# Performance work log

Hardware: AMD Instinct MI355X
Metric: run time of the kernel (lower is better)

## Reference

```python
import jax, jax.numpy as jnp
import numpy as np

EPS = 1e-5

def _relu6(x):
    return jnp.clip(x, 0.0, 6.0)

def _bn(x, g, b, m, v):
    # inference-mode batchnorm folded into scale/shift
    inv = g / jnp.sqrt(v + EPS)
    return x * inv[None, :, None, None] + (b - m * inv)[None, :, None, None]

def _patch_pw(x, W):
    # per-patch 1x1 conv. x: [B,Ci,H,Wd], W: [B,Fh,Fw,Co,Ci]
    B, C, H, Wd = x.shape
    Fh, Fw = W.shape[1:3]
    ph, pw = H // Fh, Wd // Fw
    xb = x.reshape(B, C, Fh, ph, Fw, pw)
    yb = jnp.einsum('bfgoc,bcfpgq->bofpgq', W, xb)
    return yb.reshape(B, W.shape[3], H, Wd)

def _patch_dw3(x, K):
    # per-patch depthwise 3x3, reflect pad applied to the full map (halo from neighbors).
    # x: [B,C,H,Wd], K: [B,Fh,Fw,C,3,3]
    B, C, H, Wd = x.shape
    Fh, Fw = K.shape[1:3]
    ph, pw = H // Fh, Wd // Fw
    xp = jnp.pad(x, ((0, 0), (0, 0), (1, 1), (1, 1)), mode='reflect')
    acc = jnp.zeros((B, C, Fh, ph, Fw, pw), x.dtype)
    for dy in range(3):
        for dx in range(3):
            xs = xp[:, :, dy:dy + H, dx:dx + Wd].reshape(B, C, Fh, ph, Fw, pw)
            k = K[:, :, :, :, dy, dx].transpose(0, 3, 1, 2)  # [B,C,Fh,Fw]
            acc = acc + xs * k[:, :, :, None, :, None]
    return acc.reshape(B, C, H, Wd)

def setup_inputs() -> dict:
    key = jax.random.key(0)
    ks = jax.random.split(key, 16)
    B, Cin, H, Wd = 4, 64, 128, 128
    hidden, Cout, Fh, Fw = 384, 64, 16, 16
    n_params = hidden * Cin + hidden * 9 + Cout * hidden  # 52608
    return {
        'x': jax.random.normal(ks[0], (B, Cin, H, Wd), jnp.float32),
        'w': jax.random.normal(ks[1], (B, n_params, Fh, Fw), jnp.float32) * 0.05,
        'g1': jax.random.uniform(ks[2], (hidden,), jnp.float32),
        'b1': jax.random.normal(ks[3], (hidden,), jnp.float32),
        'm1': jax.random.normal(ks[4], (hidden,), jnp.float32),
        'v1': jax.random.uniform(ks[5], (hidden,), jnp.float32),
        'g2': jax.random.uniform(ks[6], (hidden,), jnp.float32),
        'b2': jax.random.normal(ks[7], (hidden,), jnp.float32),
        'm2': jax.random.normal(ks[8], (hidden,), jnp.float32),
        'v2': jax.random.uniform(ks[9], (hidden,), jnp.float32),
        'g3': jax.random.uniform(ks[10], (Cout,), jnp.float32),
        'b3': jax.random.normal(ks[11], (Cout,), jnp.float32),
        'm3': jax.random.normal(ks[12], (Cout,), jnp.float32),
        'v3': jax.random.uniform(ks[13], (Cout,), jnp.float32),
    }

def reference(x, w, g1, b1, m1, v1, g2, b2, m2, v2, g3, b3, m3, v3):
    B, Cin = x.shape[:2]
    Fh, Fw = w.shape[2:]
    hidden = g1.shape[0]
    Cout = g3.shape[0]
    n1 = hidden * Cin
    n2 = hidden * 9
    wg = w.transpose(0, 2, 3, 1)  # [B,Fh,Fw,P]
    W1 = wg[..., :n1].reshape(B, Fh, Fw, hidden, Cin)
    K2 = wg[..., n1:n1 + n2].reshape(B, Fh, Fw, hidden, 3, 3)
    W3 = wg[..., n1 + n2:].reshape(B, Fh, Fw, Cout, hidden)
    h = _relu6(_bn(_patch_pw(x, W1), g1, b1, m1, v1))
    h = _relu6(_bn(_patch_dw3(h, K2), g2, b2, m2, v2))
    h = _bn(_patch_pw(h, W3), g3, b3, m3, v3)
    return x + h  # use_res_connect: stride==1 and in_nc==out_nc
```

## Files before the change

kernel.cpp:

```cpp
#include <hip/hip_runtime.h>

#define EPSV 1e-5f

constexpr int CIN = 64, NH = 128, NW = 128, HID = 384, COUT = 64;
constexpr int N1 = HID * CIN;
constexpr int N2 = HID * 9;
constexpr int NP = N1 + N2 + COUT * HID;

using bf16x8 = __attribute__((ext_vector_type(8))) short;
using f32x4  = __attribute__((ext_vector_type(4))) float;
using h16x2  = __attribute__((ext_vector_type(2))) _Float16;
using f16x8  = __attribute__((ext_vector_type(8))) _Float16;

__device__ __forceinline__ unsigned short f2bf(float f) {
  unsigned int u = __float_as_uint(f);
  u = (u + 0x7fffu + ((u >> 16) & 1u)) >> 16;
  return (unsigned short)u;
}
__device__ __forceinline__ unsigned int pack2(float a, float b) {
  return (unsigned int)f2bf(a) | ((unsigned int)f2bf(b) << 16);
}
__device__ __forceinline__ unsigned int pkh2(float a, float b) {
  auto h = __builtin_amdgcn_cvt_pkrtz(a, b);
  return *reinterpret_cast<unsigned int*>(&h);
}
__device__ __forceinline__ unsigned short f2h(float f) {
  _Float16 h = (_Float16)f;
  return *reinterpret_cast<unsigned short*>(&h);
}
__device__ __forceinline__ h16x2 uh2(unsigned int u) {
  return *reinterpret_cast<h16x2*>(&u);
}
__device__ __forceinline__ float clamp6(float v) { return fminf(fmaxf(v, 0.f), 6.f); }

#define BAR_LDS()                                             \
  do {                                                        \
    asm volatile("s_waitcnt lgkmcnt(0)" ::: "memory");        \
    __builtin_amdgcn_s_barrier();                             \
  } while (0)

__global__ __launch_bounds__(256) void k0_transpose(
    const float* __restrict__ x, unsigned short* __restrict__ xT) {
  __shared__ unsigned short xls[64][66];
  const int t = threadIdx.x;
  const int xh = blockIdx.x, y = blockIdx.y, b = blockIdx.z;
#pragma unroll
  for (int it = 0; it < 4; ++it) {
    int i = it * 256 + t;
    int xq = i & 15, c = i >> 4;
    float4 v = *reinterpret_cast<const float4*>(
        &x[((size_t)(b * CIN + c) * NH + y) * NW + xh * 64 + xq * 4]);
    *(unsigned int*)&xls[c][xq * 4]     = pack2(v.x, v.y);
    *(unsigned int*)&xls[c][xq * 4 + 2] = pack2(v.z, v.w);
  }
  __syncthreads();
#pragma unroll
  for (int it = 0; it < 4; ++it) {
    int i = it * 256 + t;
    int cq = i & 15, px = i >> 4;
    ushort4 o;
    o.x = xls[cq * 4 + 0][px];
    o.y = xls[cq * 4 + 1][px];
    o.z = xls[cq * 4 + 2][px];
    o.w = xls[cq * 4 + 3][px];
    *reinterpret_cast<ushort4*>(
        &xT[((size_t)(b * NH + y) * NW + xh * 64 + px) * 64 + cq * 4]) = o;
  }
}

__global__ __launch_bounds__(256) void k1_pw1(
    const float* __restrict__ w, const unsigned short* __restrict__ xT,
    const float* __restrict__ g1, const float* __restrict__ b1,
    const float* __restrict__ m1, const float* __restrict__ v1,
    unsigned short* __restrict__ h1T) {
  __shared__ unsigned short Wpk[2048 * 8];

  const unsigned int id = blockIdx.x;
  const int fbq = id & 7;
  const unsigned int rest = id >> 3;
  const int hgrp = rest % 24, q = rest / 24;
  const int fb = q * 8 + fbq;
  const int f = fb & 15, b = fb >> 4;
  const int h0 = hgrp * 16;

  const int t = threadIdx.x;
  const int lane = t & 63, wv = t >> 6;
  const int quad = lane >> 4, nn = lane & 15;
  const int pxi = wv * 16 + nn;

#pragma unroll
  for (int it = 0; it < 8; ++it) {
    int i = it * 256 + t;
    int gq = i & 3, cp = (i >> 2) & 31, hid = i >> 7;
    const float* wp =
        &w[((size_t)b * NP + (h0 + hid) * CIN + cp * 2) * 256 + f * 16 + gq * 4];
    float4 A  = *reinterpret_cast<const float4*>(wp);
    float4 Bv = *reinterpret_cast<const float4*>(wp + 256);
    int kc = cp >> 4, qd = (cp >> 2) & 3, j = (cp & 3) * 2;
    int hs = hid ^ (2 * qd) ^ gq;
    const float* Af = (const float*)&A;
    const float* Bf = (const float*)&Bv;
#pragma unroll
    for (int k = 0; k < 4; ++k) {
      int g = gq * 4 + k;
      *(unsigned int*)&Wpk[(((g * 2 + kc) * 4 + qd) * 16 + hs) * 8 + j] =
          pack2(Af[k], Bf[k]);
    }
  }

  float iv1[4], sh1[4];
#pragma unroll
  for (int jj = 0; jj < 4; ++jj) {
    int hid = h0 + quad * 4 + jj;
    float iv = g1[hid] * rsqrtf(v1[hid] + EPSV);
    iv1[jj] = iv;
    sh1[jj] = b1[hid] - m1[hid] * iv;
  }
  __syncthreads();

  const int y = f * 8 + (pxi >> 3);
  const size_t rowbase = ((size_t)b * NH + y) * NW;

  for (int g = 0; g < 16; ++g) {
    const int xc = g * 8 + (pxi & 7);
    const unsigned short* xp = &xT[(rowbase + xc) * 64];
    f32x4 acc = {0.f, 0.f, 0.f, 0.f};
    const int hs = nn ^ (2 * quad) ^ (g >> 2);
#pragma unroll
    for (int kc = 0; kc < 2; ++kc) {
      bf16x8 af = *reinterpret_cast<const bf16x8*>(
          &Wpk[(((g * 2 + kc) * 4 + quad) * 16 + hs) * 8]);
      bf16x8 bfr = *reinterpret_cast<const bf16x8*>(&xp[kc * 32 + quad * 8]);
      acc = __builtin_amdgcn_mfma_f32_16x16x32_bf16(af, bfr, acc, 0, 0, 0);
    }
    uint2 o;
    o.x = pkh2(clamp6(acc[0] * iv1[0] + sh1[0]),
               clamp6(acc[1] * iv1[1] + sh1[1]));
    o.y = pkh2(clamp6(acc[2] * iv1[2] + sh1[2]),
               clamp6(acc[3] * iv1[3] + sh1[3]));
    *reinterpret_cast<uint2*>(&h1T[(rowbase + xc) * HID + h0 + quad * 4]) = o;
  }
}

__global__ __launch_bounds__(256, 2) void k2_fused(
    const float* __restrict__ x, const float* __restrict__ w,
    const float* __restrict__ g2, const float* __restrict__ b2v,
    const float* __restrict__ m2, const float* __restrict__ v2,
    const float* __restrict__ g3, const float* __restrict__ b3v,
    const float* __restrict__ m3, const float* __restrict__ v3,
    const unsigned short* __restrict__ h1T, float* __restrict__ out) {
  __shared__ unsigned short tile[10][34][40];
  __shared__ unsigned short h2s[256][40];
  __shared__ unsigned short W3p[512 * 8];
  __shared__ unsigned short k2w[4][9][40];
  __shared__ float iv2s[HID], sh2s[HID];

  const unsigned int id = blockIdx.x;
  const int fbq = id & 7;
  const unsigned int rest = id >> 3;
  const int gang = rest & 7, q = rest >> 3;
  const int fb = q * 8 + fbq;
  const int f = fb & 15, b = fb >> 4;
  const int gq = gang >> 1, ch = gang & 1;
  const int c0 = gq * 32;

  const int t = threadIdx.x;
  const int lane = t & 63, wv = t >> 6;
  const int quad = lane >> 4, nn = lane & 15;

  for (int i = t; i < HID; i += 256) {
    float iv = g2[i] * rsqrtf(v2[i] + EPSV);
    iv2s[i] = iv;
    sh2s[i] = b2v[i] - m2[i] * iv;
  }

  float iv3[2][4], sh3[2][4];
#pragma unroll
  for (int cot = 0; cot < 2; ++cot)
#pragma unroll
    for (int jj = 0; jj < 4; ++jj) {
      int co = ch * 32 + cot * 16 + quad * 4 + jj;
      float iv = g3[co] * rsqrtf(v3[co] + EPSV);
      iv3[cot][jj] = iv;
      sh3[cot][jj] = b3v[co] - m3[co] * iv;
    }

  f32x4 acc[2][4];
#pragma unroll
  for (int cot = 0; cot < 2; ++cot)
#pragma unroll
    for (int nt = 0; nt < 4; ++nt) acc[cot][nt] = (f32x4){0.f, 0.f, 0.f, 0.f};

  const int glt = t >> 6, rt = (t >> 3) & 7, ct = t & 7;

#define TGEOM(IDX, SRC, DST)                                          \
  {                                                                   \
    int qh = (IDX) & 3, pxid = (IDX) >> 2;                            \
    int r = pxid / 34, col = pxid - r * 34;                           \
    int yy = f * 8 - 1 + r;                                           \
    yy = (yy < 0) ? -yy : ((yy > 127) ? 254 - yy : yy);               \
    int xc = c0 - 1 + col;                                            \
    xc = (xc < 0) ? 1 : ((xc > 127) ? 126 : xc);                      \
    SRC = &h1T[(((size_t)b * NH + yy) * NW + xc) * HID + qh * 8];     \
    DST = &tile[r][col][qh * 8];                                      \
  }
  const unsigned short *ts0, *ts1, *ts2, *ts3, *ts4, *ts5;
  unsigned short *td0, *td1, *td2, *td3, *td4, *td5;
  const bool tac5 = (t < 80);
  TGEOM(t, ts0, td0);
  TGEOM(256 + t, ts1, td1);
  TGEOM(512 + t, ts2, td2);
  TGEOM(768 + t, ts3, td3);
  TGEOM(1024 + t, ts4, td4);
  {
    int idx5 = tac5 ? (1280 + t) : 1359;
    TGEOM(idx5, ts5, td5);
  }
#undef TGEOM

  const int hh1 = t / 9, tap1 = t - hh1 * 9;
  const float* ksrc1 = &w[((size_t)b * NP + N1 + t) * 256 + f * 16 + gq * 4];
  const bool kac2 = (t < 32);
  const int i2k = 256 + t;
  const int hh2 = i2k / 9, tap2 = i2k - hh2 * 9;
  const float* ksrc2 = &w[((size_t)b * NP + N1 + i2k) * 256 + f * 16 + gq * 4];

  const float *wsrc0, *wsrc1;
  unsigned int *wd00, *wd01, *wd02, *wd03, *wd10, *wd11, *wd12, *wd13;
#define W3GEOM(IT, SRC, D0, D1, D2, D3)                                   \
  {                                                                      \
    int i = (IT) * 256 + t;                                              \
    int hhp = i & 15, co = i >> 4;                                       \
    SRC = &w[((size_t)b * NP + N1 + N2 + (ch * 32 + co) * HID + hhp * 2) * \
                 256 + f * 16 + gq * 4];                                 \
    int qd = (hhp * 2) >> 3, j = (hhp * 2) & 7, cot = co >> 4,           \
        cb = co & 15;                                                    \
    D0 = (unsigned int*)&W3p[(((0 * 2 + cot) * 4 + qd) * 16 +            \
                              (cb ^ (2 * qd) ^ 0)) * 8 + j];             \
    D1 = (unsigned int*)&W3p[(((1 * 2 + cot) * 4 + qd) * 16 +            \
                              (cb ^ (2 * qd) ^ 1)) * 8 + j];             \
    D2 = (unsigned int*)&W3p[(((2 * 2 + cot) * 4 + qd) * 16 +            \
                              (cb ^ (2 * qd) ^ 2)) * 8 + j];             \
    D3 = (unsigned int*)&W3p[(((3 * 2 + cot) * 4 + qd) * 16 +            \
                              (cb ^ (2 * qd) ^ 3)) * 8 + j];             \
  }
  W3GEOM(0, wsrc0, wd00, wd01, wd02, wd03);
  W3GEOM(1, wsrc1, wd10, wd11, wd12, wd13);
#undef W3GEOM

  uint4 tr0, tr1, tr2, tr3, tr4, tr5;
  float4 kr1, kr2;
  float4 wA0, wB0, wA1, wB1;

#define PREFETCH()                                                  \
  do {                                                              \
    tr0 = *reinterpret_cast<const uint4*>(ts0); ts0 += 32;          \
    tr1 = *reinterpret_cast<const uint4*>(ts1); ts1 += 32;          \
    tr2 = *reinterpret_cast<const uint4*>(ts2); ts2 += 32;          \
    tr3 = *reinterpret_cast<const uint4*>(ts3); ts3 += 32;          \
    tr4 = *reinterpret_cast<const uint4*>(ts4); ts4 += 32;          \
    if (tac5) tr5 = *reinterpret_cast<const uint4*>(ts5);           \
    ts5 += 32;                                                      \
    kr1 = *reinterpret_cast<const float4*>(ksrc1); ksrc1 += 73728;  \
    if (kac2) kr2 = *reinterpret_cast<const float4*>(ksrc2);        \
    ksrc2 += 73728;                                                 \
    wA0 = *reinterpret_cast<const float4*>(wsrc0);                  \
    wB0 = *reinterpret_cast<const float4*>(wsrc0 + 256);            \
    wsrc0 += 8192;                                                  \
    wA1 = *reinterpret_cast<const float4*>(wsrc1);                  \
    wB1 = *reinterpret_cast<const float4*>(wsrc1 + 256);            \
    wsrc1 += 8192;                                                  \
  } while (0)

  tr5 = (uint4){0u, 0u, 0u, 0u};
  kr2 = (float4){0.f, 0.f, 0.f, 0.f};
  PREFETCH();

  const h16x2 hz = {(_Float16)0.f, (_Float16)0.f};

  for (int hc = 0; hc < 12; ++hc) {
    const int hb = hc * 32;
    BAR_LDS();

    *reinterpret_cast<uint4*>(td0) = tr0;
    *reinterpret_cast<uint4*>(td1) = tr1;
    *reinterpret_cast<uint4*>(td2) = tr2;
    *reinterpret_cast<uint4*>(td3) = tr3;
    *reinterpret_cast<uint4*>(td4) = tr4;
    if (tac5) *reinterpret_cast<uint4*>(td5) = tr5;
    k2w[0][tap1][hh1] = f2h(kr1.x);
    k2w[1][tap1][hh1] = f2h(kr1.y);
    k2w[2][tap1][hh1] = f2h(kr1.z);
    k2w[3][tap1][hh1] = f2h(kr1.w);
    if (kac2) {
      k2w[0][tap2][hh2] = f2h(kr2.x);
      k2w[1][tap2][hh2] = f2h(kr2.y);
      k2w[2][tap2][hh2] = f2h(kr2.z);
      k2w[3][tap2][hh2] = f2h(kr2.w);
    }
    *wd00 = pkh2(wA0.x, wB0.x);
    *wd01 = pkh2(wA0.y, wB0.y);
    *wd02 = pkh2(wA0.z, wB0.z);
    *wd03 = pkh2(wA0.w, wB0.w);
    *wd10 = pkh2(wA1.x, wB1.x);
    *wd11 = pkh2(wA1.y, wB1.y);
    *wd12 = pkh2(wA1.z, wB1.z);
    *wd13 = pkh2(wA1.w, wB1.w);

    BAR_LDS();

    if (hc < 11) PREFETCH();

#pragma unroll
    for (int hg = 0; hg < 4; ++hg) {
      h16x2 d0 = hz, d1 = hz, d2 = hz, d3 = hz;
#pragma unroll
      for (int dy = 0; dy < 3; ++dy)
#pragma unroll
        for (int dx = 0; dx < 3; ++dx) {
          const uint4 tv = *reinterpret_cast<const uint4*>(
              &tile[rt + dy][glt * 8 + ct + dx][hg * 8]);
          const uint4 kv =
              *reinterpret_cast<const uint4*>(&k2w[glt][dy * 3 + dx][hg * 8]);
          d0 += uh2(tv.x) * uh2(kv.x);
          d1 += uh2(tv.y) * uh2(kv.y);
          d2 += uh2(tv.z) * uh2(kv.z);
          d3 += uh2(tv.w) * uh2(kv.w);
        }
      const int ha = hb + hg * 8;
      uint4 o4;
      o4.x = pkh2(clamp6((float)d0[0] * iv2s[ha + 0] + sh2s[ha + 0]),
                  clamp6((float)d0[1] * iv2s[ha + 1] + sh2s[ha + 1]));
      o4.y = pkh2(clamp6((float)d1[0] * iv2s[ha + 2] + sh2s[ha + 2]),
                  clamp6((float)d1[1] * iv2s[ha + 3] + sh2s[ha + 3]));
      o4.z = pkh2(clamp6((float)d2[0] * iv2s[ha + 4] + sh2s[ha + 4]),
                  clamp6((float)d2[1] * iv2s[ha + 5] + sh2s[ha + 5]));
      o4.w = pkh2(clamp6((float)d3[0] * iv2s[ha + 6] + sh2s[ha + 6]),
                  clamp6((float)d3[1] * iv2s[ha + 7] + sh2s[ha + 7]));
      *reinterpret_cast<uint4*>(&h2s[t][hg * 8]) = o4;
    }

    BAR_LDS();

    {
      const int gl = wv;
      const int cop = nn ^ (2 * quad) ^ gl;
      f16x8 a0 = *reinterpret_cast<const f16x8*>(
          &W3p[(((gl * 2 + 0) * 4 + quad) * 16 + cop) * 8]);
      f16x8 a1 = *reinterpret_cast<const f16x8*>(
          &W3p[(((gl * 2 + 1) * 4 + quad) * 16 + cop) * 8]);
#pragma unroll
      for (int nt = 0; nt < 4; ++nt) {
        f16x8 bfr = *reinterpret_cast<const f16x8*>(
            &h2s[gl * 64 + nt * 16 + nn][quad * 8]);
        acc[0][nt] = __builtin_amdgcn_mfma_f32_16x16x32_f16(a0, bfr, acc[0][nt], 0, 0, 0);
        acc[1][nt] = __builtin_amdgcn_mfma_f32_16x16x32_f16(a1, bfr, acc[1][nt], 0, 0, 0);
      }
    }
  }

#pragma unroll
  for (int cot = 0; cot < 2; ++cot)
#pragma unroll
    for (int nt = 0; nt < 4; ++nt) {
      int pxl = nt * 16 + nn;
      int y = f * 8 + (pxl >> 3);
      int xc = c0 + wv * 8 + (pxl & 7);
#pragma unroll
      for (int jj = 0; jj < 4; ++jj) {
        int co = ch * 32 + cot * 16 + quad * 4 + jj;
        size_t adr = ((size_t)(b * COUT + co) * NH + y) * NW + xc;
        out[adr] = acc[cot][nt][jj] * iv3[cot][jj] + sh3[cot][jj] + x[adr];
      }
    }
}

extern "C" void kernel_launch(void* const* d_in, const int* in_sizes, int n_in,
                              void* d_out, int out_size, void* d_ws,
                              size_t ws_size, hipStream_t stream) {
  (void)in_sizes; (void)n_in; (void)out_size; (void)ws_size;
  const float* x  = (const float*)d_in[0];
  const float* w  = (const float*)d_in[1];
  const float* g1 = (const float*)d_in[2];
  const float* b1 = (const float*)d_in[3];
  const float* m1 = (const float*)d_in[4];
  const float* v1 = (const float*)d_in[5];
  const float* g2 = (const float*)d_in[6];
  const float* b2 = (const float*)d_in[7];
  const float* m2 = (const float*)d_in[8];
  const float* v2 = (const float*)d_in[9];
  const float* g3 = (const float*)d_in[10];
  const float* b3 = (const float*)d_in[11];
  const float* m3 = (const float*)d_in[12];
  const float* v3 = (const float*)d_in[13];
  float* out = (float*)d_out;
  unsigned short* h1T = (unsigned short*)d_ws;
  unsigned short* xT = (unsigned short*)d_out;

  k0_transpose<<<dim3(2, 128, 4), 256, 0, stream>>>(x, xT);
  k1_pw1<<<dim3(1536), 256, 0, stream>>>(w, xT, g1, b1, m1, v1, h1T);
  k2_fused<<<dim3(512), 256, 0, stream>>>(x, w, g2, b2, m2, v2, g3, b3, m3, v3,
                                          h1T, out);
}
```

Measured before the change: 431.3 us.

## Split k2 block work by spatial rows instead of output channels

Each k2 block now covers a 4-row by 32-column pixel tile and computes all 64 output channels, where before it covered an 8x32 tile and only half the channels. The depthwise 3x3 stage is no longer done twice for the same pixels, and the halo tile and h2s buffers shrink. Each block now stages the full W3 slice (twice as much per block) and has proportionally more halo overhead. LDS use drops enough that launch bounds are raised from 2 to 3 blocks per SIMD for occupancy.

```diff
diff --git a/kernel.cpp b/kernel.cpp
--- a/kernel.cpp
+++ b/kernel.cpp
@@ -142,16 +142,16 @@
   }
 }
 
-__global__ __launch_bounds__(256, 2) void k2_fused(
+__global__ __launch_bounds__(256, 3) void k2_fused(
     const float* __restrict__ x, const float* __restrict__ w,
     const float* __restrict__ g2, const float* __restrict__ b2v,
     const float* __restrict__ m2, const float* __restrict__ v2,
     const float* __restrict__ g3, const float* __restrict__ b3v,
     const float* __restrict__ m3, const float* __restrict__ v3,
     const unsigned short* __restrict__ h1T, float* __restrict__ out) {
-  __shared__ unsigned short tile[10][34][40];
-  __shared__ unsigned short h2s[256][40];
-  __shared__ unsigned short W3p[512 * 8];
+  __shared__ unsigned short tile[6][34][40];
+  __shared__ unsigned short h2s[128][40];
+  __shared__ unsigned short W3p[8192];
   __shared__ unsigned short k2w[4][9][40];
   __shared__ float iv2s[HID], sh2s[HID];
 
@@ -163,10 +163,14 @@
   const int f = fb & 15, b = fb >> 4;
   const int gq = gang >> 1, ch = gang & 1;
   const int c0 = gq * 32;
+  const int r0 = f * 8 + ch * 4;
 
   const int t = threadIdx.x;
   const int lane = t & 63, wv = t >> 6;
   const int quad = lane >> 4, nn = lane & 15;
+  const int glh = wv & 1, coh = wv >> 1;
+  const int p = t & 127, hhalf = t >> 7;
+  const int patchq = p >> 5, prt = (p >> 3) & 3, pct = p & 7;
 
   for (int i = t; i < HID; i += 256) {
     float iv = g2[i] * rsqrtf(v2[i] + EPSV);
@@ -179,7 +183,7 @@
   for (int cot = 0; cot < 2; ++cot)
 #pragma unroll
     for (int jj = 0; jj < 4; ++jj) {
-      int co = ch * 32 + cot * 16 + quad * 4 + jj;
+      int co = coh * 32 + cot * 16 + quad * 4 + jj;
       float iv = g3[co] * rsqrtf(v3[co] + EPSV);
       iv3[cot][jj] = iv;
       sh3[cot][jj] = b3v[co] - m3[co] * iv;
@@ -190,31 +194,27 @@
   for (int cot = 0; cot < 2; ++cot)
 #pragma unroll
     for (int nt = 0; nt < 4; ++nt) acc[cot][nt] = (f32x4){0.f, 0.f, 0.f, 0.f};
-
-  const int glt = t >> 6, rt = (t >> 3) & 7, ct = t & 7;
 
 #define TGEOM(IDX, SRC, DST)                                          \
   {                                                                   \
     int qh = (IDX) & 3, pxid = (IDX) >> 2;                            \
     int r = pxid / 34, col = pxid - r * 34;                           \
-    int yy = f * 8 - 1 + r;                                           \
+    int yy = r0 - 1 + r;                                              \
     yy = (yy < 0) ? -yy : ((yy > 127) ? 254 - yy : yy);               \
     int xc = c0 - 1 + col;                                            \
     xc = (xc < 0) ? 1 : ((xc > 127) ? 126 : xc);                      \
     SRC = &h1T[(((size_t)b * NH + yy) * NW + xc) * HID + qh * 8];     \
     DST = &tile[r][col][qh * 8];                                      \
   }
-  const unsigned short *ts0, *ts1, *ts2, *ts3, *ts4, *ts5;
-  unsigned short *td0, *td1, *td2, *td3, *td4, *td5;
-  const bool tac5 = (t < 80);
+  const unsigned short *ts0, *ts1, *ts2, *ts3;
+  unsigned short *td0, *td1, *td2, *td3;
+  const bool tac3 = (t < 48);
   TGEOM(t, ts0, td0);
   TGEOM(256 + t, ts1, td1);
   TGEOM(512 + t, ts2, td2);
-  TGEOM(768 + t, ts3, td3);
-  TGEOM(1024 + t, ts4, td4);
   {
-    int idx5 = tac5 ? (1280 + t) : 1359;
-    TGEOM(idx5, ts5, td5);
+    int idx3 = tac3 ? (768 + t) : 815;
+    TGEOM(idx3, ts3, td3);
   }
 #undef TGEOM
 
@@ -225,42 +225,37 @@
   const int hh2 = i2k / 9, tap2 = i2k - hh2 * 9;
   const float* ksrc2 = &w[((size_t)b * NP + N1 + i2k) * 256 + f * 16 + gq * 4];
 
-  const float *wsrc0, *wsrc1;
-  unsigned int *wd00, *wd01, *wd02, *wd03, *wd10, *wd11, *wd12, *wd13;
-#define W3GEOM(IT, SRC, D0, D1, D2, D3)                                   \
+  const float *wsrc0, *wsrc1, *wsrc2, *wsrc3;
+  unsigned int wb0, wb1, wb2, wb3;
+#define W3GEOM(IT, SRC, WB)                                               \
   {                                                                      \
     int i = (IT) * 256 + t;                                              \
-    int hhp = i & 15, co = i >> 4;                                       \
-    SRC = &w[((size_t)b * NP + N1 + N2 + (ch * 32 + co) * HID + hhp * 2) * \
-                 256 + f * 16 + gq * 4];                                 \
-    int qd = (hhp * 2) >> 3, j = (hhp * 2) & 7, cot = co >> 4,           \
-        cb = co & 15;                                                    \
-    D0 = (unsigned int*)&W3p[(((0 * 2 + cot) * 4 + qd) * 16 +            \
-                              (cb ^ (2 * qd) ^ 0)) * 8 + j];             \
-    D1 = (unsigned int*)&W3p[(((1 * 2 + cot) * 4 + qd) * 16 +            \
-                              (cb ^ (2 * qd) ^ 1)) * 8 + j];             \
-    D2 = (unsigned int*)&W3p[(((2 * 2 + cot) * 4 + qd) * 16 +            \
-                              (cb ^ (2 * qd) ^ 2)) * 8 + j];             \
-    D3 = (unsigned int*)&W3p[(((3 * 2 + cot) * 4 + qd) * 16 +            \
-                              (cb ^ (2 * qd) ^ 3)) * 8 + j];             \
-  }
-  W3GEOM(0, wsrc0, wd00, wd01, wd02, wd03);
-  W3GEOM(1, wsrc1, wd10, wd11, wd12, wd13);
+    int hhp = i & 15, co = i >> 4;                         \
+    SRC = &w[((size_t)b * NP + N1 + N2 + co * HID + hhp * 2) * 256 +     \
+             f * 16 + gq * 4];                                           \
+    int qd = (hhp * 2) >> 3, j = (hhp * 2) & 7;                          \
+    int ch2 = co >> 5, cot = (co >> 4) & 1, cb = co & 15;                \
+    int cop0 = cb ^ (2 * qd);                                            \
+    WB = (unsigned int)(ch2 * 8192 + (cot * 4 + qd) * 256 + cop0 * 16 +  \
+                        j * 2);                                          \
+  }
+  W3GEOM(0, wsrc0, wb0);
+  W3GEOM(1, wsrc1, wb1);
+  W3GEOM(2, wsrc2, wb2);
+  W3GEOM(3, wsrc3, wb3);
 #undef W3GEOM
 
-  uint4 tr0, tr1, tr2, tr3, tr4, tr5;
+  uint4 tr0, tr1, tr2, tr3;
   float4 kr1, kr2;
-  float4 wA0, wB0, wA1, wB1;
+  float4 wA0, wB0, wA1, wB1, wA2, wB2, wA3, wB3;
 
 #define PREFETCH()                                                  \
   do {                                                              \
     tr0 = *reinterpret_cast<const uint4*>(ts0); ts0 += 32;          \
     tr1 = *reinterpret_cast<const uint4*>(ts1); ts1 += 32;          \
     tr2 = *reinterpret_cast<const uint4*>(ts2); ts2 += 32;          \
-    tr3 = *reinterpret_cast<const uint4*>(ts3); ts3 += 32;          \
-    tr4 = *reinterpret_cast<const uint4*>(ts4); ts4 += 32;          \
-    if (tac5) tr5 = *reinterpret_cast<const uint4*>(ts5);           \
-    ts5 += 32;                                                      \
+    if (tac3) tr3 = *reinterpret_cast<const uint4*>(ts3);           \
+    ts3 += 32;                                                      \
     kr1 = *reinterpret_cast<const float4*>(ksrc1); ksrc1 += 73728;  \
     if (kac2) kr2 = *reinterpret_cast<const float4*>(ksrc2);        \
     ksrc2 += 73728;                                                 \
@@ -270,9 +265,25 @@
     wA1 = *reinterpret_cast<const float4*>(wsrc1);                  \
     wB1 = *reinterpret_cast<const float4*>(wsrc1 + 256);            \
     wsrc1 += 8192;                                                  \
+    wA2 = *reinterpret_cast<const float4*>(wsrc2);                  \
+    wB2 = *reinterpret_cast<const float4*>(wsrc2 + 256);            \
+    wsrc2 += 8192;                                                  \
+    wA3 = *reinterpret_cast<const float4*>(wsrc3);                  \
+    wB3 = *reinterpret_cast<const float4*>(wsrc3 + 256);            \
+    wsrc3 += 8192;                                                  \
   } while (0)
 
-  tr5 = (uint4){0u, 0u, 0u, 0u};
+#define W3WRITE(WB, WA, WV)                                                   \
+  do {                                                                        \
+    const float* Af = (const float*)&(WA);                                    \
+    const float* Bf = (const float*)&(WV);                                    \
+    *(unsigned int*)((char*)W3p + (WB))                  = pkh2(Af[0], Bf[0]);\
+    *(unsigned int*)((char*)W3p + (((WB) ^ 16) + 2048))  = pkh2(Af[1], Bf[1]);\
+    *(unsigned int*)((char*)W3p + (((WB) ^ 32) + 4096))  = pkh2(Af[2], Bf[2]);\
+    *(unsigned int*)((char*)W3p + (((WB) ^ 48) + 6144))  = pkh2(Af[3], Bf[3]);\
+  } while (0)
+
+  tr3 = (uint4){0u, 0u, 0u, 0u};
   kr2 = (float4){0.f, 0.f, 0.f, 0.f};
   PREFETCH();
 
@@ -285,9 +296,7 @@
     *reinterpret_cast<uint4*>(td0) = tr0;
     *reinterpret_cast<uint4*>(td1) = tr1;
     *reinterpret_cast<uint4*>(td2) = tr2;
-    *reinterpret_cast<uint4*>(td3) = tr3;
-    *reinterpret_cast<uint4*>(td4) = tr4;
-    if (tac5) *reinterpret_cast<uint4*>(td5) = tr5;
+    if (tac3) *reinterpret_cast<uint4*>(td3) = tr3;
     k2w[0][tap1][hh1] = f2h(kr1.x);
     k2w[1][tap1][hh1] = f2h(kr1.y);
     k2w[2][tap1][hh1] = f2h(kr1.z);
@@ -298,30 +307,27 @@
       k2w[2][tap2][hh2] = f2h(kr2.z);
       k2w[3][tap2][hh2] = f2h(kr2.w);
     }
-    *wd00 = pkh2(wA0.x, wB0.x);
-    *wd01 = pkh2(wA0.y, wB0.y);
-    *wd02 = pkh2(wA0.z, wB0.z);
-    *wd03 = pkh2(wA0.w, wB0.w);
-    *wd10 = pkh2(wA1.x, wB1.x);
-    *wd11 = pkh2(wA1.y, wB1.y);
-    *wd12 = pkh2(wA1.z, wB1.z);
-    *wd13 = pkh2(wA1.w, wB1.w);
+    W3WRITE(wb0, wA0, wB0);
+    W3WRITE(wb1, wA1, wB1);
+    W3WRITE(wb2, wA2, wB2);
+    W3WRITE(wb3, wA3, wB3);
 
     BAR_LDS();
 
     if (hc < 11) PREFETCH();
 
 #pragma unroll
-    for (int hg = 0; hg < 4; ++hg) {
+    for (int hg2 = 0; hg2 < 2; ++hg2) {
+      const int hg = hhalf * 2 + hg2;
       h16x2 d0 = hz, d1 = hz, d2 = hz, d3 = hz;
 #pragma unroll
       for (int dy = 0; dy < 3; ++dy)
 #pragma unroll
         for (int dx = 0; dx < 3; ++dx) {
           const uint4 tv = *reinterpret_cast<const uint4*>(
-              &tile[rt + dy][glt * 8 + ct + dx][hg * 8]);
+              &tile[prt + dy][patchq * 8 + pct + dx][hg * 8]);
           const uint4 kv =
-              *reinterpret_cast<const uint4*>(&k2w[glt][dy * 3 + dx][hg * 8]);
+              *reinterpret_cast<const uint4*>(&k2w[patchq][dy * 3 + dx][hg * 8]);
           d0 += uh2(tv.x) * uh2(kv.x);
           d1 += uh2(tv.y) * uh2(kv.y);
           d2 += uh2(tv.z) * uh2(kv.z);
@@ -337,24 +343,33 @@
                   clamp6((float)d2[1] * iv2s[ha + 5] + sh2s[ha + 5]));
       o4.w = pkh2(clamp6((float)d3[0] * iv2s[ha + 6] + sh2s[ha + 6]),
                   clamp6((float)d3[1] * iv2s[ha + 7] + sh2s[ha + 7]));
-      *reinterpret_cast<uint4*>(&h2s[t][hg * 8]) = o4;
+      *reinterpret_cast<uint4*>(&h2s[p][hg * 8]) = o4;
     }
 
     BAR_LDS();
 
     {
-      const int gl = wv;
-      const int cop = nn ^ (2 * quad) ^ gl;
-      f16x8 a0 = *reinterpret_cast<const f16x8*>(
-          &W3p[(((gl * 2 + 0) * 4 + quad) * 16 + cop) * 8]);
-      f16x8 a1 = *reinterpret_cast<const f16x8*>(
-          &W3p[(((gl * 2 + 1) * 4 + quad) * 16 + cop) * 8]);
+      const int cop0 = nn ^ (2 * quad);
+      const int kp0 = glh * 2, kp1 = glh * 2 + 1;
+      f16x8 aA0 = *reinterpret_cast<const f16x8*>(
+          &W3p[coh * 4096 + (((kp0 * 2 + 0) * 4 + quad) * 16 + (cop0 ^ kp0)) * 8]);
+      f16x8 aB0 = *reinterpret_cast<const f16x8*>(
+          &W3p[coh * 4096 + (((kp0 * 2 + 1) * 4 + quad) * 16 + (cop0 ^ kp0)) * 8]);
+      f16x8 aA1 = *reinterpret_cast<const f16x8*>(
+          &W3p[coh * 4096 + (((kp1 * 2 + 0) * 4 + quad) * 16 + (cop0 ^ kp1)) * 8]);
+      f16x8 aB1 = *reinterpret_cast<const f16x8*>(
+          &W3p[coh * 4096 + (((kp1 * 2 + 1) * 4 + quad) * 16 + (cop0 ^ kp1)) * 8]);
 #pragma unroll
       for (int nt = 0; nt < 4; ++nt) {
         f16x8 bfr = *reinterpret_cast<const f16x8*>(
-            &h2s[gl * 64 + nt * 16 + nn][quad * 8]);
-        acc[0][nt] = __builtin_amdgcn_mfma_f32_16x16x32_f16(a0, bfr, acc[0][nt], 0, 0, 0);
-        acc[1][nt] = __builtin_amdgcn_mfma_f32_16x16x32_f16(a1, bfr, acc[1][nt], 0, 0, 0);
+            &h2s[glh * 64 + nt * 16 + nn][quad * 8]);
+        if (nt < 2) {
+          acc[0][nt] = __builtin_amdgcn_mfma_f32_16x16x32_f16(aA0, bfr, acc[0][nt], 0, 0, 0);
+          acc[1][nt] = __builtin_amdgcn_mfma_f32_16x16x32_f16(aB0, bfr, acc[1][nt], 0, 0, 0);
+        } else {
+          acc[0][nt] = __builtin_amdgcn_mfma_f32_16x16x32_f16(aA1, bfr, acc[0][nt], 0, 0, 0);
+          acc[1][nt] = __builtin_amdgcn_mfma_f32_16x16x32_f16(aB1, bfr, acc[1][nt], 0, 0, 0);
+        }
       }
     }
   }
@@ -363,12 +378,13 @@
   for (int cot = 0; cot < 2; ++cot)
 #pragma unroll
     for (int nt = 0; nt < 4; ++nt) {
-      int pxl = nt * 16 + nn;
-      int y = f * 8 + (pxl >> 3);
-      int xc = c0 + wv * 8 + (pxl & 7);
+      int rt_ = (nt & 1) * 2 + (nn >> 3);
+      int patch_ = glh * 2 + (nt >> 1);
+      int y = r0 + rt_;
+      int xc = c0 + patch_ * 8 + (nn & 7);
 #pragma unroll
       for (int jj = 0; jj < 4; ++jj) {
-        int co = ch * 32 + cot * 16 + quad * 4 + jj;
+        int co = coh * 32 + cot * 16 + quad * 4 + jj;
         size_t adr = ((size_t)(b * COUT + co) * NH + y) * NW + xc;
         out[adr] = acc[cot][nt][jj] * iv3[cot][jj] + sh3[cot][jj] + x[adr];
       }
```

Measured after the change: 479.9 us. 1.11x slower.
